# Performance work log

Measured on AMD Instinct MI355X. Metric: run time of the kernel, lower is better.

## Reference

```python
import jax, jax.numpy as jnp
import numpy as np

EPS = 1e-5

def _layernorm(x, gamma, beta):
    mu = x.mean(-1, keepdims=True)
    var = ((x - mu) ** 2).mean(-1, keepdims=True)
    return (x - mu) * jax.lax.rsqrt(var + EPS) * gamma + beta

def setup_inputs() -> dict:
    key = jax.random.key(0)
    k1, k2, k3, k4, k5 = jax.random.split(key, 5)
    V, P, IN, H, OUT = 200000, 32, 4, 16, 16
    B, GH, GW, GZ = 1, 512, 512, 32
    features = jax.random.normal(k1, (V, P, IN), dtype=jnp.float32)
    num_points = jax.random.randint(k2, (V,), 1, P + 1, dtype=jnp.int32)
    # unique voxel coordinates: distinct linear indices decomposed into (b,ix,iy,iz)
    total = B * GH * GW * GZ
    stride = total // V  # >=1, so arange(V)*stride are distinct and in-range
    lin = jnp.arange(V, dtype=jnp.int32) * stride
    iz = lin % GZ
    iy = (lin // GZ) % GW
    ix = (lin // (GZ * GW)) % GH
    b = lin // (GZ * GW * GH)
    coords = jnp.stack([b, ix, iy, iz], axis=1).astype(jnp.int32)
    # parameters (kaiming-ish small init)
    W1 = jax.random.normal(k3, (IN, H), dtype=jnp.float32) * 0.5
    b1 = jnp.zeros((H,), jnp.float32)
    g1 = jnp.ones((H,), jnp.float32)
    be1 = jnp.zeros((H,), jnp.float32)
    W2 = jax.random.normal(k4, (H, OUT), dtype=jnp.float32) * 0.25
    b2 = jnp.zeros((OUT,), jnp.float32)
    g2 = jnp.ones((OUT,), jnp.float32)
    be2 = jnp.zeros((OUT,), jnp.float32)
    return {"features": features, "num_points": num_points, "coords": coords,
            "W1": W1, "b1": b1, "g1": g1, "be1": be1,
            "W2": W2, "b2": b2, "g2": g2, "be2": be2,
            "batch_size": B, "grid_h": GH, "grid_w": GW, "grid_z": GZ}

def reference(features, num_points, coords, W1, b1, g1, be1, W2, b2, g2, be2,
              batch_size, grid_h, grid_w, grid_z):
    V, P, _ = features.shape
    mask = (jnp.arange(P)[None, :] < num_points[:, None]).astype(features.dtype)  # (V,P)
    h = _layernorm(features @ W1 + b1, g1, be1)          # (V,P,H)
    h = jax.nn.relu(h)
    x = h @ W2 + b2                                      # (V,P,OUT)
    x = (x * mask[:, :, None]).sum(axis=1)               # masked sum pool -> (V,OUT)
    x = _layernorm(x, g2, be2)                           # (V,OUT)
    dense = jnp.zeros((batch_size, grid_h, grid_w, grid_z, x.shape[-1]), x.dtype)
    bi, ix, iy, iz = coords[:, 0], coords[:, 1], coords[:, 2], coords[:, 3]
    return dense.at[bi, ix, iy, iz].set(x, mode="drop")
```

## Files before the change

kernel.cpp:

```cpp
#include <hip/hip_runtime.h>

__global__ void __launch_bounds__(256)
voxel_pointnet_kernel(
    const float* __restrict__ features,
    const int* __restrict__ num_points,
    const int* __restrict__ coords,
    const float* __restrict__ W1, const float* __restrict__ b1,
    const float* __restrict__ g1, const float* __restrict__ be1,
    const float* __restrict__ W2, const float* __restrict__ b2,
    const float* __restrict__ g2, const float* __restrict__ be2,
    const int* __restrict__ pB, const int* __restrict__ pGH,
    const int* __restrict__ pGW, const int* __restrict__ pGZ,
    float* __restrict__ out, int V, int P)
{
    __shared__ float sW1[64], sb1[16], sg1[16], sbe1[16];
    __shared__ float sW2[256], sb2[16], sg2[16], sbe2[16];
    int t = threadIdx.x;
    if (t < 64)  sW1[t] = W1[t];
    if (t < 256) sW2[t] = W2[t];
    if (t < 16) {
        sb1[t] = b1[t]; sg1[t] = g1[t]; sbe1[t] = be1[t];
        sb2[t] = b2[t]; sg2[t] = g2[t]; sbe2[t] = be2[t];
    }
    __syncthreads();

    int v = blockIdx.x * blockDim.x + t;
    if (v >= V) return;

    int np = num_points[v];
    np = np < 0 ? 0 : (np > P ? P : np);

    float hsum[16];
    #pragma unroll
    for (int j = 0; j < 16; j++) hsum[j] = 0.f;

    const float4* fp = (const float4*)(features + (size_t)v * P * 4);

    float4 f = (np > 0) ? fp[0] : make_float4(0.f, 0.f, 0.f, 0.f);
    for (int p = 0; p < np; p++) {
        float4 fnext;
        if (p + 1 < np) fnext = fp[p + 1];
        float h[16];
        float mu = 0.f;
        #pragma unroll
        for (int j = 0; j < 16; j++) {
            float acc = sb1[j];
            acc = fmaf(f.x, sW1[j],      acc);
            acc = fmaf(f.y, sW1[16 + j], acc);
            acc = fmaf(f.z, sW1[32 + j], acc);
            acc = fmaf(f.w, sW1[48 + j], acc);
            h[j] = acc;
            mu += acc;
        }
        mu *= 0.0625f;
        float var = 0.f;
        #pragma unroll
        for (int j = 0; j < 16; j++) { float d = h[j] - mu; var = fmaf(d, d, var); }
        var *= 0.0625f;
        float r = rsqrtf(var + 1e-5f);
        #pragma unroll
        for (int j = 0; j < 16; j++) {
            float val = fmaf((h[j] - mu) * r, sg1[j], sbe1[j]);
            hsum[j] += fmaxf(val, 0.f);
        }
        f = fnext;
    }

    float fn = (float)np;
    float x[16];
    float mu = 0.f;
    #pragma unroll
    for (int j = 0; j < 16; j++) {
        float acc = fn * sb2[j];
        #pragma unroll
        for (int k = 0; k < 16; k++) acc = fmaf(hsum[k], sW2[k * 16 + j], acc);
        x[j] = acc;
        mu += acc;
    }
    mu *= 0.0625f;
    float var = 0.f;
    #pragma unroll
    for (int j = 0; j < 16; j++) { float d = x[j] - mu; var = fmaf(d, d, var); }
    var *= 0.0625f;
    float r = rsqrtf(var + 1e-5f);
    #pragma unroll
    for (int j = 0; j < 16; j++) x[j] = fmaf((x[j] - mu) * r, sg2[j], sbe2[j]);

    int B = *pB, GH = *pGH, GW = *pGW, GZ = *pGZ;
    int4 c = *(const int4*)(coords + (size_t)v * 4);
    if ((unsigned)c.x >= (unsigned)B || (unsigned)c.y >= (unsigned)GH ||
        (unsigned)c.z >= (unsigned)GW || (unsigned)c.w >= (unsigned)GZ) return;

    size_t o = ((((size_t)c.x * GH + c.y) * GW + c.z) * GZ + c.w) * 16;
    float4* op = (float4*)(out + o);
    op[0] = make_float4(x[0],  x[1],  x[2],  x[3]);
    op[1] = make_float4(x[4],  x[5],  x[6],  x[7]);
    op[2] = make_float4(x[8],  x[9],  x[10], x[11]);
    op[3] = make_float4(x[12], x[13], x[14], x[15]);
}

extern "C" void kernel_launch(void* const* d_in, const int* in_sizes, int n_in,
                              void* d_out, int out_size, void* d_ws, size_t ws_size,
                              hipStream_t stream) {
    const float* features = (const float*)d_in[0];
    const int*   num_points = (const int*)d_in[1];
    const int*   coords   = (const int*)d_in[2];
    const float* W1  = (const float*)d_in[3];
    const float* b1  = (const float*)d_in[4];
    const float* g1  = (const float*)d_in[5];
    const float* be1 = (const float*)d_in[6];
    const float* W2  = (const float*)d_in[7];
    const float* b2  = (const float*)d_in[8];
    const float* g2  = (const float*)d_in[9];
    const float* be2 = (const float*)d_in[10];
    const int* pB  = (const int*)d_in[11];
    const int* pGH = (const int*)d_in[12];
    const int* pGW = (const int*)d_in[13];
    const int* pGZ = (const int*)d_in[14];
    float* out = (float*)d_out;

    int V  = in_sizes[1];
    int IN = in_sizes[3] / in_sizes[4];
    int P  = in_sizes[0] / (V * IN);

    hipMemsetAsync(d_out, 0, (size_t)out_size * sizeof(float), stream);

    int blocks = (V + 255) / 256;
    voxel_pointnet_kernel<<<blocks, 256, 0, stream>>>(
        features, num_points, coords, W1, b1, g1, be1, W2, b2, g2, be2,
        pB, pGH, pGW, pGZ, out, V, P);
}
```

Measured before the change: 655.8 us.

## Overlap output zeroing with voxel compute in one kernel, then scatter

Result: slower. 669.5 us (+2.1%).

```diff
diff --git a/kernel.cpp b/kernel.cpp
--- a/kernel.cpp
+++ b/kernel.cpp
@@ -1,7 +1,134 @@
 #include <hip/hip_runtime.h>
 
+
+#define ZBLOCKS 1024
+
 __global__ void __launch_bounds__(256)
-voxel_pointnet_kernel(
+fused_zero_compute_kernel(
+    const float* __restrict__ features,
+    const int* __restrict__ num_points,
+    const int* __restrict__ coords,
+    const float* __restrict__ W1, const float* __restrict__ b1,
+    const float* __restrict__ g1, const float* __restrict__ be1,
+    const float* __restrict__ W2, const float* __restrict__ b2,
+    const float* __restrict__ g2, const float* __restrict__ be2,
+    const int* __restrict__ pB, const int* __restrict__ pGH,
+    const int* __restrict__ pGW, const int* __restrict__ pGZ,
+    float* __restrict__ out, long long n4out,
+    float* __restrict__ wsx, int* __restrict__ wsoff,
+    int V, int P, int vblocks)
+{
+    if ((int)blockIdx.x >= vblocks) {
+        long long i = (long long)(blockIdx.x - vblocks) * blockDim.x + threadIdx.x;
+        long long stride = (long long)(gridDim.x - vblocks) * blockDim.x;
+        float4 z = make_float4(0.f, 0.f, 0.f, 0.f);
+        float4* o4 = (float4*)out;
+        for (; i < n4out; i += stride) o4[i] = z;
+        return;
+    }
+
+    __shared__ float sW1[64], sb1[16], sg1[16], sbe1[16];
+    __shared__ float sW2[256], sb2[16], sg2[16], sbe2[16];
+    int t = threadIdx.x;
+    if (t < 64)  sW1[t] = W1[t];
+    if (t < 256) sW2[t] = W2[t];
+    if (t < 16) {
+        sb1[t] = b1[t]; sg1[t] = g1[t]; sbe1[t] = be1[t];
+        sb2[t] = b2[t]; sg2[t] = g2[t]; sbe2[t] = be2[t];
+    }
+    __syncthreads();
+
+    int v = blockIdx.x * blockDim.x + t;
+    if (v >= V) return;
+
+    int np = num_points[v];
+    np = np < 0 ? 0 : (np > P ? P : np);
+
+    float hsum[16];
+    #pragma unroll
+    for (int j = 0; j < 16; j++) hsum[j] = 0.f;
+
+    const float4* fp = (const float4*)(features + (size_t)v * P * 4);
+    float4 f = (np > 0) ? fp[0] : make_float4(0.f, 0.f, 0.f, 0.f);
+    for (int p = 0; p < np; p++) {
+        float4 fnext;
+        if (p + 1 < np) fnext = fp[p + 1];
+        float h[16];
+        float mu = 0.f;
+        #pragma unroll
+        for (int j = 0; j < 16; j++) {
+            float acc = sb1[j];
+            acc = fmaf(f.x, sW1[j],      acc);
+            acc = fmaf(f.y, sW1[16 + j], acc);
+            acc = fmaf(f.z, sW1[32 + j], acc);
+            acc = fmaf(f.w, sW1[48 + j], acc);
+            h[j] = acc;
+            mu += acc;
+        }
+        mu *= 0.0625f;
+        float var = 0.f;
+        #pragma unroll
+        for (int j = 0; j < 16; j++) { float d = h[j] - mu; var = fmaf(d, d, var); }
+        var *= 0.0625f;
+        float r = rsqrtf(var + 1e-5f);
+        #pragma unroll
+        for (int j = 0; j < 16; j++) {
+            float val = fmaf((h[j] - mu) * r, sg1[j], sbe1[j]);
+            hsum[j] += fmaxf(val, 0.f);
+        }
+        f = fnext;
+    }
+
+    float fn = (float)np;
+    float x[16];
+    float mu = 0.f;
+    #pragma unroll
+    for (int j = 0; j < 16; j++) {
+        float acc = fn * sb2[j];
+        #pragma unroll
+        for (int k = 0; k < 16; k++) acc = fmaf(hsum[k], sW2[k * 16 + j], acc);
+        x[j] = acc;
+        mu += acc;
+    }
+    mu *= 0.0625f;
+    float var = 0.f;
+    #pragma unroll
+    for (int j = 0; j < 16; j++) { float d = x[j] - mu; var = fmaf(d, d, var); }
+    var *= 0.0625f;
+    float r = rsqrtf(var + 1e-5f);
+    #pragma unroll
+    for (int j = 0; j < 16; j++) x[j] = fmaf((x[j] - mu) * r, sg2[j], sbe2[j]);
+
+    float4* wx = (float4*)(wsx + (size_t)v * 16);
+    wx[0] = make_float4(x[0],  x[1],  x[2],  x[3]);
+    wx[1] = make_float4(x[4],  x[5],  x[6],  x[7]);
+    wx[2] = make_float4(x[8],  x[9],  x[10], x[11]);
+    wx[3] = make_float4(x[12], x[13], x[14], x[15]);
+
+    int B = *pB, GH = *pGH, GW = *pGW, GZ = *pGZ;
+    int4 c = *(const int4*)(coords + (size_t)v * 4);
+    int off = -1;
+    if ((unsigned)c.x < (unsigned)B && (unsigned)c.y < (unsigned)GH &&
+        (unsigned)c.z < (unsigned)GW && (unsigned)c.w < (unsigned)GZ) {
+        off = (int)(((((size_t)c.x * GH + c.y) * GW + c.z) * GZ + c.w) * 16);
+    }
+    wsoff[v] = off;
+}
+
+__global__ void __launch_bounds__(256)
+scatter_kernel(const float* __restrict__ wsx, const int* __restrict__ wsoff,
+               float* __restrict__ out, int V)
+{
+    int idx = blockIdx.x * blockDim.x + threadIdx.x;
+    int v = idx >> 2, part = idx & 3;
+    if (v >= V) return;
+    int off = wsoff[v];
+    if (off < 0) return;
+    ((float4*)(out + (size_t)off))[part] = ((const float4*)(wsx + (size_t)v * 16))[part];
+}
+
+__global__ void __launch_bounds__(256)
+voxel_pointnet_direct_kernel(
     const float* __restrict__ features,
     const int* __restrict__ num_points,
     const int* __restrict__ coords,
@@ -23,23 +150,16 @@
         sb2[t] = b2[t]; sg2[t] = g2[t]; sbe2[t] = be2[t];
     }
     __syncthreads();
-
     int v = blockIdx.x * blockDim.x + t;
     if (v >= V) return;
-
     int np = num_points[v];
     np = np < 0 ? 0 : (np > P ? P : np);
-
     float hsum[16];
     #pragma unroll
     for (int j = 0; j < 16; j++) hsum[j] = 0.f;
-
     const float4* fp = (const float4*)(features + (size_t)v * P * 4);
-
-    float4 f = (np > 0) ? fp[0] : make_float4(0.f, 0.f, 0.f, 0.f);
     for (int p = 0; p < np; p++) {
-        float4 fnext;
-        if (p + 1 < np) fnext = fp[p + 1];
+        float4 f = fp[p];
         float h[16];
         float mu = 0.f;
         #pragma unroll
@@ -49,8 +169,7 @@
             acc = fmaf(f.y, sW1[16 + j], acc);
             acc = fmaf(f.z, sW1[32 + j], acc);
             acc = fmaf(f.w, sW1[48 + j], acc);
-            h[j] = acc;
-            mu += acc;
+            h[j] = acc; mu += acc;
         }
         mu *= 0.0625f;
         float var = 0.f;
@@ -63,19 +182,15 @@
             float val = fmaf((h[j] - mu) * r, sg1[j], sbe1[j]);
             hsum[j] += fmaxf(val, 0.f);
         }
-        f = fnext;
-    }
-
+    }
     float fn = (float)np;
-    float x[16];
-    float mu = 0.f;
+    float x[16]; float mu = 0.f;
     #pragma unroll
     for (int j = 0; j < 16; j++) {
         float acc = fn * sb2[j];
         #pragma unroll
         for (int k = 0; k < 16; k++) acc = fmaf(hsum[k], sW2[k * 16 + j], acc);
-        x[j] = acc;
-        mu += acc;
+        x[j] = acc; mu += acc;
     }
     mu *= 0.0625f;
     float var = 0.f;
@@ -85,12 +200,10 @@
     float r = rsqrtf(var + 1e-5f);
     #pragma unroll
     for (int j = 0; j < 16; j++) x[j] = fmaf((x[j] - mu) * r, sg2[j], sbe2[j]);
-
     int B = *pB, GH = *pGH, GW = *pGW, GZ = *pGZ;
     int4 c = *(const int4*)(coords + (size_t)v * 4);
     if ((unsigned)c.x >= (unsigned)B || (unsigned)c.y >= (unsigned)GH ||
         (unsigned)c.z >= (unsigned)GW || (unsigned)c.w >= (unsigned)GZ) return;
-
     size_t o = ((((size_t)c.x * GH + c.y) * GW + c.z) * GZ + c.w) * 16;
     float4* op = (float4*)(out + o);
     op[0] = make_float4(x[0],  x[1],  x[2],  x[3]);
@@ -123,10 +236,23 @@
     int IN = in_sizes[3] / in_sizes[4];
     int P  = in_sizes[0] / (V * IN);
 
-    hipMemsetAsync(d_out, 0, (size_t)out_size * sizeof(float), stream);
-
-    int blocks = (V + 255) / 256;
-    voxel_pointnet_kernel<<<blocks, 256, 0, stream>>>(
-        features, num_points, coords, W1, b1, g1, be1, W2, b2, g2, be2,
-        pB, pGH, pGW, pGZ, out, V, P);
-}
+    long long n4 = (long long)out_size / 4;
+    size_t ws_need = (size_t)V * 16 * sizeof(float) + (size_t)V * sizeof(int);
+
+    if (ws_size >= ws_need) {
+        float* wsx = (float*)d_ws;
+        int*   wsoff = (int*)((char*)d_ws + (size_t)V * 16 * sizeof(float));
+        int vblocks = (V + 255) / 256;
+        fused_zero_compute_kernel<<<vblocks + ZBLOCKS, 256, 0, stream>>>(
+            features, num_points, coords, W1, b1, g1, be1, W2, b2, g2, be2,
+            pB, pGH, pGW, pGZ, out, n4, wsx, wsoff, V, P, vblocks);
+        int sblocks = (V * 4 + 255) / 256;
+        scatter_kernel<<<sblocks, 256, 0, stream>>>(wsx, wsoff, out, V);
+    } else {
+        hipMemsetAsync(d_out, 0, (size_t)out_size * sizeof(float), stream);
+        int blocks = (V + 255) / 256;
+        voxel_pointnet_direct_kernel<<<blocks, 256, 0, stream>>>(
+            features, num_points, coords, W1, b1, g1, be1, W2, b2, g2, be2,
+            pB, pGH, pGW, pGZ, out, V, P);
+    }
+}
```
